# Kernel tuning notes

Measured on AMD Instinct MI355X. Metric: run time of the kernel, lower is better.

The kernel has to match this reference:

```python
import jax, jax.numpy as jnp
import numpy as np

NUM_HEADS = 8
HEAD_DIM = 128
ATTN_SCALE = 0.12


def _rotary_tables(T, head_dim, dtype=jnp.float32):
    # modded-nanogpt half-truncated RoPE: rotate only first half of freq slots
    quarter = head_dim // 4
    angular = (1.0 / 1024.0) ** jnp.linspace(0.0, 1.0, quarter, dtype=dtype)
    angular = jnp.concatenate([angular, jnp.zeros(quarter, dtype=dtype)])  # [head_dim//2]
    t = jnp.arange(T, dtype=dtype)
    theta = t[:, None] * angular[None, :]  # [T, head_dim//2]
    return jnp.cos(theta), jnp.sin(theta)


def _apply_rotary(x, cos, sin):
    # x: [B, T, H, D]; cos/sin: [T, D//2]
    x1, x2 = jnp.split(x, 2, axis=-1)
    c = cos[None, :, None, :]
    s = sin[None, :, None, :]
    y1 = x1 * c + x2 * s
    y2 = -x1 * s + x2 * c
    return jnp.concatenate([y1, y2], axis=-1)


def _rms_norm(x):
    eps = jnp.asarray(jnp.finfo(x.dtype).eps, x.dtype)
    var = jnp.mean(jnp.square(x), axis=-1, keepdims=True)
    return x * jax.lax.rsqrt(var + eps)


def setup_inputs() -> dict:
    key = jax.random.key(0)
    k1, k2, k3, k4, k5 = jax.random.split(key, 5)
    B, T, D = 1, 4096, 1024
    hdim = NUM_HEADS * HEAD_DIM
    std = 0.5 * D ** (-0.5)
    x = jax.random.normal(k1, (B, T, D), dtype=jnp.float32)
    ve = jax.random.normal(k2, (B, T, hdim), dtype=jnp.float32)
    qkv_w = jax.random.normal(k3, (3, hdim, D), dtype=jnp.float32) * std
    lambdas = jnp.array([0.5, 0.5], dtype=jnp.float32)
    c_proj_w = jax.random.normal(k5, (D, hdim), dtype=jnp.float32) * std
    return {"x": x, "ve": ve, "qkv_w": qkv_w, "lambdas": lambdas, "c_proj_w": c_proj_w}


def reference(x, ve, qkv_w, lambdas, c_proj_w):
    B, T, D = x.shape
    H, Hd = NUM_HEADS, HEAD_DIM
    # QKV projection: qkv_w [3, H*Hd, D]
    qkv = jnp.einsum('btd,ckd->btck', x, qkv_w)  # [B, T, 3, H*Hd]
    qkv = qkv.reshape(B, T, 3, H, Hd)
    q, k, v = qkv[:, :, 0], qkv[:, :, 1], qkv[:, :, 2]  # [B, T, H, Hd]
    # QK RMSNorm
    q = _rms_norm(q)
    k = _rms_norm(k)
    # RoPE
    cos, sin = _rotary_tables(T, Hd, dtype=x.dtype)
    q = _apply_rotary(q, cos, sin)
    k = _apply_rotary(k, cos, sin)
    # value-embedding lambda mix
    v = lambdas[0] * v + lambdas[1] * ve.reshape(B, T, H, Hd)
    # causal attention with fixed scale 0.12 (block-causal FlexAttention mask)
    scores = jnp.einsum('bthd,bshd->bhts', q, k) * ATTN_SCALE  # [B, H, T, T]
    causal = jnp.tril(jnp.ones((T, T), dtype=bool))
    scores = jnp.where(causal[None, None], scores, jnp.asarray(-jnp.inf, scores.dtype))
    probs = jax.nn.softmax(scores, axis=-1)
    y = jnp.einsum('bhts,bshd->bthd', probs, v)  # [B, T, H, Hd]
    y = y.reshape(B, T, H * Hd)
    return y @ c_proj_w.T  # [B, T, D]
```

## Files before the change

### kernel.cpp

```cpp
#include <hip/hip_runtime.h>

typedef __bf16 bf16;
typedef __bf16 bf16x8 __attribute__((ext_vector_type(8)));
typedef __bf16 bf16x4 __attribute__((ext_vector_type(4)));
typedef __bf16 bf16x2 __attribute__((ext_vector_type(2)));
typedef float f32x4 __attribute__((ext_vector_type(4)));
typedef float f32x16 __attribute__((ext_vector_type(16)));
typedef int i32x4 __attribute__((ext_vector_type(4)));

#define GLL16(gp, lp)                                                          \
  __builtin_amdgcn_global_load_lds(                                            \
      (const __attribute__((address_space(1))) unsigned int*)(gp),             \
      (__attribute__((address_space(3))) unsigned int*)(lp), 16, 0, 0)

__global__ __launch_bounds__(256) void cast3_f32_bf16(
    const float* __restrict__ a, bf16* __restrict__ oa, int na4,
    const float* __restrict__ b, bf16* __restrict__ ob, int nb4,
    const float* __restrict__ c, bf16* __restrict__ oc, int nc4) {
  int i = blockIdx.x * blockDim.x + threadIdx.x;
  int stride = gridDim.x * blockDim.x;
  int total = na4 + nb4 + nc4;
  for (; i < total; i += stride) {
    const float4* src;
    bf16x4* dst;
    int j = i;
    if (j < na4) {
      src = (const float4*)a + j; dst = (bf16x4*)oa + j;
    } else if ((j -= na4) < nb4) {
      src = (const float4*)b + j; dst = (bf16x4*)ob + j;
    } else {
      j -= nb4;
      src = (const float4*)c + j; dst = (bf16x4*)oc + j;
    }
    float4 v = *src;
    bf16x4 o;
    o[0] = (bf16)v.x; o[1] = (bf16)v.y; o[2] = (bf16)v.z; o[3] = (bf16)v.w;
    *dst = o;
  }
}

template <int K, int LDC, typename CT>
__global__ __launch_bounds__(256) void gemm_bt(
    const bf16* __restrict__ A, const bf16* __restrict__ B,
    CT* __restrict__ C) {
  __shared__ __align__(16) bf16 As[128 * 64];
  __shared__ __align__(16) bf16 Bs[128 * 64];
  const int tid  = threadIdx.x;
  const int lane = tid & 63;
  const int wave = tid >> 6;
  const int ln15 = lane & 15, quad = lane >> 4;
  const int wm = wave >> 1, wn = wave & 1;
  const int m0 = blockIdx.y * 128, n0 = blockIdx.x * 128;

  f32x4 acc[4][4] = {};

  for (int k0 = 0; k0 < K; k0 += 64) {
    __syncthreads();
#pragma unroll
    for (int j = 0; j < 4; ++j) {
      int gbase = j * 256 + wave * 64;
      int g = gbase + lane;
      int r = g >> 3, c = (g & 7) ^ (r & 7);
      GLL16(A + (size_t)(m0 + r) * K + k0 + c * 8, As + (size_t)gbase * 8);
    }
#pragma unroll
    for (int j = 0; j < 4; ++j) {
      int gbase = j * 256 + wave * 64;
      int g = gbase + lane;
      int r = g >> 3, c = (g & 7) ^ (r & 7);
      GLL16(B + (size_t)(n0 + r) * K + k0 + c * 8, Bs + (size_t)gbase * 8);
    }
    __syncthreads();
#pragma unroll
    for (int kk = 0; kk < 2; ++kk) {
      bf16x8 af[4], bfr[4];
#pragma unroll
      for (int mi = 0; mi < 4; ++mi) {
        int m = wm * 64 + mi * 16 + ln15;
        int cg = kk * 4 + quad;
        af[mi] = *(const bf16x8*)(As + (m * 8 + (cg ^ (m & 7))) * 8);
      }
#pragma unroll
      for (int ni = 0; ni < 4; ++ni) {
        int n = wn * 64 + ni * 16 + ln15;
        int cg = kk * 4 + quad;
        bfr[ni] = *(const bf16x8*)(Bs + (n * 8 + (cg ^ (n & 7))) * 8);
      }
#pragma unroll
      for (int mi = 0; mi < 4; ++mi)
#pragma unroll
        for (int ni = 0; ni < 4; ++ni)
          acc[mi][ni] = __builtin_amdgcn_mfma_f32_16x16x32_bf16(
              af[mi], bfr[ni], acc[mi][ni], 0, 0, 0);
    }
  }
#pragma unroll
  for (int mi = 0; mi < 4; ++mi)
#pragma unroll
    for (int ni = 0; ni < 4; ++ni)
#pragma unroll
      for (int r = 0; r < 4; ++r) {
        int row = m0 + wm * 64 + mi * 16 + quad * 4 + r;
        int col = n0 + wn * 64 + ni * 16 + ln15;
        C[(size_t)row * LDC + col] = (CT)acc[mi][ni][r];
      }
}

__global__ __launch_bounds__(256) void qkv_post(
    const bf16* __restrict__ qkv, const float* __restrict__ ve,
    const float* __restrict__ lambdas, bf16* __restrict__ qn,
    bf16* __restrict__ kn, bf16* __restrict__ vt) {
  const int h  = blockIdx.x;
  const int t0 = blockIdx.y * 64;
  const int tid = threadIdx.x;
  const int wave = tid >> 6, lane = tid & 63;
  __shared__ __align__(16) float tile[64][129];

  const int j = lane;
  float cth = 1.0f, sth = 0.0f;
  for (int i = 0; i < 16; ++i) {
    int t = t0 + wave * 16 + i;
    if (j < 32) {
      float ang = exp2f((float)j * (-10.0f / 31.0f));
      float th = (float)t * ang;
      __sincosf(th, &sth, &cth);
    }
#pragma unroll
    for (int qk = 0; qk < 2; ++qk) {
      const bf16* row = qkv + (size_t)t * 3072 + qk * 1024 + h * 128;
      float x1 = (float)row[j], x2 = (float)row[j + 64];
      float ss = x1 * x1 + x2 * x2;
#pragma unroll
      for (int m = 1; m < 64; m <<= 1) ss += __shfl_xor(ss, m, 64);
      float rinv = rsqrtf(ss * (1.0f / 128.0f) + 1.1920929e-7f);
      if (qk == 0) rinv *= 0.12f;
      float y1 = (x1 * cth + x2 * sth) * rinv;
      float y2 = (x2 * cth - x1 * sth) * rinv;
      bf16* orow = (qk == 0 ? qn : kn) + (size_t)t * 1024 + h * 128;
      orow[j] = (bf16)y1;
      orow[j + 64] = (bf16)y2;
    }
  }

  float l0 = lambdas[0], l1 = lambdas[1];
  for (int c = 0; c < 32; ++c) {
    int idx = c * 256 + tid;
    int d = idx & 127, tl = idx >> 7;
    int t = t0 + tl;
    float v = (float)qkv[(size_t)t * 3072 + 2048 + h * 128 + d];
    float vev = ve[(size_t)t * 1024 + h * 128 + d];
    tile[tl][d] = l0 * v + l1 * vev;
  }
  __syncthreads();
  for (int c = 0; c < 32; ++c) {
    int idx = c * 256 + tid;
    int tl = idx & 63, d = idx >> 6;
    vt[((size_t)(h * 128 + d)) * 4096 + t0 + tl] = (bf16)tile[tl][d];
  }
}

__global__ __launch_bounds__(256, 2) void flash_attn(
    const bf16* __restrict__ qn, const bf16* __restrict__ kn,
    const bf16* __restrict__ vt, bf16* __restrict__ y) {
  const int halfg = blockIdx.x >> 8;
  const int idx = blockIdx.x & 255;
  const int h = idx & 7;
  const int p = idx >> 3;
  const int qtile = halfg ? p : 63 - p;
  const int tid = threadIdx.x;
  const int wave = tid >> 6, lane = tid & 63;
  const int l31 = lane & 31, hl = lane >> 5;
  const int qi = wave >> 1, ki = wave & 1;

  __shared__ __align__(16) bf16 Ks[2][64 * 128];
  __shared__ __align__(16) bf16 Vs[2][128 * 64];
  __shared__ float rsb[2][2][32];

  const int q0 = qtile * 64;
  const int nkv = qtile + 1;
  const int qg = q0 + qi * 32 + l31;

  bf16x8 qf[8];
  {
    const bf16* qb = qn + (size_t)qg * 1024 + h * 128 + hl * 8;
#pragma unroll
    for (int f = 0; f < 8; ++f) qf[f] = *(const bf16x8*)(qb + f * 16);
  }

  f32x16 acc_o[4] = {};
  float rs = 0.0f;

  auto prefetch = [&](int kt, int buf) {
    const int kv0 = kt * 64;
    bf16* ks = &Ks[buf][0];
    bf16* vs = &Vs[buf][0];
#pragma unroll
    for (int jj = 0; jj < 4; ++jj) {
      int gbase = jj * 256 + wave * 64;
      int g = gbase + lane;
      int r = g >> 4, c = (g & 15) ^ (r & 15);
      GLL16(kn + (size_t)(kv0 + r) * 1024 + h * 128 + c * 8,
            ks + (size_t)gbase * 8);
    }
#pragma unroll
    for (int jj = 0; jj < 4; ++jj) {
      int gbase = jj * 256 + wave * 64;
      int g = gbase + lane;
      int d = g >> 3, c = (g & 7) ^ (d & 7);
      GLL16(vt + ((size_t)(h * 128 + d)) * 4096 + kv0 + c * 8,
            vs + (size_t)gbase * 8);
    }
  };

  prefetch(0, 0);

  for (int kt = 0; kt < nkv; ++kt) {
    const int kv0 = kt * 64;
    __syncthreads();
    if (kt + 1 < nkv) prefetch(kt + 1, (kt + 1) & 1);
    const bf16* ksb = &Ks[kt & 1][0];
    const bf16* vsb = &Vs[kt & 1][0];

    f32x16 accs = {};
    const int krow = ki * 32 + l31;
#pragma unroll
    for (int f = 0; f < 8; ++f) {
      bf16x8 a =
          *(const bf16x8*)(ksb + (krow * 16 + ((2 * f + hl) ^ (krow & 15))) * 8);
      accs = __builtin_amdgcn_mfma_f32_32x32x16_bf16(a, qf[f], accs, 0, 0, 0);
    }

    const bool diag = (kt == nkv - 1);
    float pe[16];
#pragma unroll
    for (int r = 0; r < 16; ++r) {
      int kvl = (r & 3) + 8 * (r >> 2) + 4 * hl;
      float v = __expf(accs[r]);
      if (diag && (kv0 + ki * 32 + kvl) > qg) v = 0.0f;
      rs += v;
      pe[r] = v;
    }
    int pk[8];
#pragma unroll
    for (int g = 0; g < 8; ++g) {
      bf16x2 t;
      t[0] = (bf16)pe[2 * g];
      t[1] = (bf16)pe[2 * g + 1];
      pk[g] = __builtin_bit_cast(int, t);
    }

    bf16x8 pf[2];
#pragma unroll
    for (int c = 0; c < 2; ++c) {
      int sh0 = __shfl_xor(pk[4 * c + 0], 32, 64);
      int sh1 = __shfl_xor(pk[4 * c + 1], 32, 64);
      int sh2 = __shfl_xor(pk[4 * c + 2], 32, 64);
      int sh3 = __shfl_xor(pk[4 * c + 3], 32, 64);
      int own0 = hl ? pk[4 * c + 2] : pk[4 * c + 0];
      int own1 = hl ? pk[4 * c + 3] : pk[4 * c + 1];
      int par0 = hl ? sh2 : sh0;
      int par1 = hl ? sh3 : sh1;
      i32x4 dv;
      dv[0] = hl ? par0 : own0;
      dv[1] = hl ? par1 : own1;
      dv[2] = hl ? own0 : par0;
      dv[3] = hl ? own1 : par1;
      pf[c] = __builtin_bit_cast(bf16x8, dv);
    }

#pragma unroll
    for (int dt = 0; dt < 4; ++dt) {
      int vrow = dt * 32 + l31;
#pragma unroll
      for (int c = 0; c < 2; ++c) {
        bf16x8 a = *(const bf16x8*)(
            vsb + (vrow * 8 + ((4 * ki + 2 * c + hl) ^ (vrow & 7))) * 8);
        acc_o[dt] =
            __builtin_amdgcn_mfma_f32_32x32x16_bf16(a, pf[c], acc_o[dt], 0, 0, 0);
      }
    }
  }

  rs += __shfl_xor(rs, 32, 64);
  __syncthreads();
  if (lane < 32) rsb[qi][ki][l31] = rs;
  float* ob = (float*)&Ks[0][0];
  if (ki == 1) {
#pragma unroll
    for (int dt = 0; dt < 4; ++dt)
#pragma unroll
      for (int r = 0; r < 16; ++r) {
        int d = dt * 32 + (r & 3) + 8 * (r >> 2) + 4 * hl;
        ob[qi * 4096 + l31 * 128 + d] = acc_o[dt][r];
      }
  }
  __syncthreads();
  if (ki == 0) {
    float inv = 1.0f / (rsb[qi][0][l31] + rsb[qi][1][l31]);
#pragma unroll
    for (int dt = 0; dt < 4; ++dt)
#pragma unroll
      for (int rg = 0; rg < 4; ++rg) {
        bf16x4 o;
#pragma unroll
        for (int j = 0; j < 4; ++j) {
          int r = rg * 4 + j;
          int d = dt * 32 + 4 * hl + 8 * rg + j;
          o[j] = (bf16)((acc_o[dt][r] + ob[qi * 4096 + l31 * 128 + d]) * inv);
        }
        *(bf16x4*)(y + (size_t)qg * 1024 + h * 128 + dt * 32 + 4 * hl + 8 * rg) = o;
      }
  }
}

extern "C" void kernel_launch(void* const* d_in, const int* in_sizes, int n_in,
                              void* d_out, int out_size, void* d_ws,
                              size_t ws_size, hipStream_t stream) {
  const float* x       = (const float*)d_in[0];
  const float* ve      = (const float*)d_in[1];
  const float* qkv_w   = (const float*)d_in[2];
  const float* lambdas = (const float*)d_in[3];
  const float* c_proj  = (const float*)d_in[4];
  float* out = (float*)d_out;

  char* ws = (char*)d_ws;
  bf16* qkv   = (bf16*)ws;
  bf16* xbf   = (bf16*)(ws + 25165824);
  bf16* wqkv  = (bf16*)(ws + 33554432);
  bf16* wproj = (bf16*)(ws + 39845888);
  bf16* qn    = (bf16*)(ws + 41943040);
  bf16* kn    = (bf16*)(ws + 50331648);
  bf16* vt    = (bf16*)(ws + 58720256);
  bf16* yb    = (bf16*)(ws + 67108864);

  cast3_f32_bf16<<<2048, 256, 0, stream>>>(x, xbf, 4194304 / 4, qkv_w, wqkv,
                                           3145728 / 4, c_proj, wproj,
                                           1048576 / 4);

  gemm_bt<1024, 3072, bf16><<<dim3(24, 32), 256, 0, stream>>>(xbf, wqkv, qkv);

  qkv_post<<<dim3(8, 64), 256, 0, stream>>>(qkv, ve, lambdas, qn, kn, vt);

  flash_attn<<<512, 256, 0, stream>>>(qn, kn, vt, yb);

  gemm_bt<1024, 1024, float><<<dim3(8, 32), 256, 0, stream>>>(yb, wproj, out);
}
```

Baseline: 252.3 us.

## Split attention KV range across two blocks and combine partials in separate kernel

Each query tile's causal KV range is now split into two halves processed by separate blocks, doubling the grid, with unnormalized fp32 partial outputs and row sums written to workspace. A new combine kernel adds the two partials and normalizes into bf16. Blocks are ordered longest-first so the heavy causal tiles start early. This is meant to improve load balance and occupancy. The cost is extra fp32 global traffic, an additional launch, and reuse of workspace regions freed earlier.

```diff
diff --git a/kernel.cpp b/kernel.cpp
--- a/kernel.cpp
+++ b/kernel.cpp
@@ -161,23 +161,40 @@
 
 __global__ __launch_bounds__(256, 2) void flash_attn(
     const bf16* __restrict__ qn, const bf16* __restrict__ kn,
-    const bf16* __restrict__ vt, bf16* __restrict__ y) {
-  const int halfg = blockIdx.x >> 8;
-  const int idx = blockIdx.x & 255;
-  const int h = idx & 7;
-  const int p = idx >> 3;
-  const int qtile = halfg ? p : 63 - p;
+    const bf16* __restrict__ vt, float* __restrict__ Op,
+    float* __restrict__ ls) {
+  const int id = blockIdx.x;
+  const int qtile = 63 - (id >> 4);
+  const int sub = id & 15;
+  const int h = sub >> 1;
+  const int half = sub & 1;
   const int tid = threadIdx.x;
   const int wave = tid >> 6, lane = tid & 63;
   const int l31 = lane & 31, hl = lane >> 5;
   const int qi = wave >> 1, ki = wave & 1;
 
-  __shared__ __align__(16) bf16 Ks[2][64 * 128];
-  __shared__ __align__(16) bf16 Vs[2][128 * 64];
+  __shared__ __align__(16) bf16 smem[4 * 64 * 128];
   __shared__ float rsb[2][2][32];
+  bf16* Ks = smem;
+  bf16* Vs = smem + 2 * 64 * 128;
 
   const int q0 = qtile * 64;
   const int nkv = qtile + 1;
+  const int half0 = (nkv + 1) >> 1;
+  const int kt_begin = half ? half0 : 0;
+  const int kt_end = half ? nkv : half0;
+  const int niter = kt_end - kt_begin;
+  const int pidx = (h * 64 + qtile) * 2 + half;
+
+  if (niter == 0) {
+    float4 z = {0.f, 0.f, 0.f, 0.f};
+    float* opb = Op + (size_t)pidx * 8192;
+#pragma unroll
+    for (int j = 0; j < 8; ++j) *(float4*)(opb + tid * 32 + j * 4) = z;
+    if (tid < 64) ls[pidx * 64 + tid] = 0.f;
+    return;
+  }
+
   const int qg = q0 + qi * 32 + l31;
 
   bf16x8 qf[8];
@@ -192,8 +209,8 @@
 
   auto prefetch = [&](int kt, int buf) {
     const int kv0 = kt * 64;
-    bf16* ks = &Ks[buf][0];
-    bf16* vs = &Vs[buf][0];
+    bf16* ks = Ks + buf * (64 * 128);
+    bf16* vs = Vs + buf * (128 * 64);
 #pragma unroll
     for (int jj = 0; jj < 4; ++jj) {
       int gbase = jj * 256 + wave * 64;
@@ -212,14 +229,15 @@
     }
   };
 
-  prefetch(0, 0);
-
-  for (int kt = 0; kt < nkv; ++kt) {
+  prefetch(kt_begin, 0);
+
+  for (int it = 0; it < niter; ++it) {
+    const int kt = kt_begin + it;
     const int kv0 = kt * 64;
     __syncthreads();
-    if (kt + 1 < nkv) prefetch(kt + 1, (kt + 1) & 1);
-    const bf16* ksb = &Ks[kt & 1][0];
-    const bf16* vsb = &Vs[kt & 1][0];
+    if (it + 1 < niter) prefetch(kt + 1, (it + 1) & 1);
+    const bf16* ksb = Ks + (it & 1) * (64 * 128);
+    const bf16* vsb = Vs + (it & 1) * (128 * 64);
 
     f32x16 accs = {};
     const int krow = ki * 32 + l31;
@@ -284,33 +302,56 @@
   rs += __shfl_xor(rs, 32, 64);
   __syncthreads();
   if (lane < 32) rsb[qi][ki][l31] = rs;
-  float* ob = (float*)&Ks[0][0];
+  float* ob = (float*)smem;
   if (ki == 1) {
 #pragma unroll
     for (int dt = 0; dt < 4; ++dt)
 #pragma unroll
       for (int r = 0; r < 16; ++r) {
         int d = dt * 32 + (r & 3) + 8 * (r >> 2) + 4 * hl;
-        ob[qi * 4096 + l31 * 128 + d] = acc_o[dt][r];
+        ob[(qi * 32 + l31) * 129 + d] = acc_o[dt][r];
       }
   }
   __syncthreads();
   if (ki == 0) {
-    float inv = 1.0f / (rsb[qi][0][l31] + rsb[qi][1][l31]);
+    float lsum = rsb[qi][0][l31] + rsb[qi][1][l31];
+    if (hl == 0) ls[pidx * 64 + qi * 32 + l31] = lsum;
+    float* opb = Op + (size_t)pidx * 8192 + (qi * 32 + l31) * 128;
 #pragma unroll
     for (int dt = 0; dt < 4; ++dt)
 #pragma unroll
       for (int rg = 0; rg < 4; ++rg) {
-        bf16x4 o;
-#pragma unroll
-        for (int j = 0; j < 4; ++j) {
-          int r = rg * 4 + j;
-          int d = dt * 32 + 4 * hl + 8 * rg + j;
-          o[j] = (bf16)((acc_o[dt][r] + ob[qi * 4096 + l31 * 128 + d]) * inv);
-        }
-        *(bf16x4*)(y + (size_t)qg * 1024 + h * 128 + dt * 32 + 4 * hl + 8 * rg) = o;
-      }
-  }
+        float4 o;
+        int d0 = dt * 32 + 4 * hl + 8 * rg;
+        o.x = acc_o[dt][rg * 4 + 0] + ob[(qi * 32 + l31) * 129 + d0 + 0];
+        o.y = acc_o[dt][rg * 4 + 1] + ob[(qi * 32 + l31) * 129 + d0 + 1];
+        o.z = acc_o[dt][rg * 4 + 2] + ob[(qi * 32 + l31) * 129 + d0 + 2];
+        o.w = acc_o[dt][rg * 4 + 3] + ob[(qi * 32 + l31) * 129 + d0 + 3];
+        *(float4*)(opb + d0) = o;
+      }
+  }
+}
+
+__global__ __launch_bounds__(256) void attn_combine(
+    const float* __restrict__ Op, const float* __restrict__ ls,
+    bf16* __restrict__ y) {
+  int gid = blockIdx.x * 256 + threadIdx.x;
+  int t = gid >> 8;
+  int c4 = gid & 255;
+  int qtile = t >> 6, ql = t & 63;
+  int h = c4 >> 5;
+  int d = (c4 & 31) * 4;
+  int pbase = (h * 64 + qtile) * 2;
+  const float4 o0 = *(const float4*)(Op + (size_t)pbase * 8192 + ql * 128 + d);
+  const float4 o1 =
+      *(const float4*)(Op + (size_t)(pbase + 1) * 8192 + ql * 128 + d);
+  float inv = 1.0f / (ls[pbase * 64 + ql] + ls[(pbase + 1) * 64 + ql]);
+  bf16x4 o;
+  o[0] = (bf16)((o0.x + o1.x) * inv);
+  o[1] = (bf16)((o0.y + o1.y) * inv);
+  o[2] = (bf16)((o0.z + o1.z) * inv);
+  o[3] = (bf16)((o0.w + o1.w) * inv);
+  *(bf16x4*)(y + (size_t)t * 1024 + h * 128 + d) = o;
 }
 
 extern "C" void kernel_launch(void* const* d_in, const int* in_sizes, int n_in,
@@ -332,6 +373,8 @@
   bf16* kn    = (bf16*)(ws + 50331648);
   bf16* vt    = (bf16*)(ws + 58720256);
   bf16* yb    = (bf16*)(ws + 67108864);
+  float* Op  = (float*)ws;
+  float* lsw = (float*)(ws + 33554432);
 
   cast3_f32_bf16<<<2048, 256, 0, stream>>>(x, xbf, 4194304 / 4, qkv_w, wqkv,
                                            3145728 / 4, c_proj, wproj,
@@ -341,7 +384,8 @@
 
   qkv_post<<<dim3(8, 64), 256, 0, stream>>>(qkv, ve, lambdas, qn, kn, vt);
 
-  flash_attn<<<512, 256, 0, stream>>>(qn, kn, vt, yb);
+  flash_attn<<<1024, 256, 0, stream>>>(qn, kn, vt, Op, lsw);
+  attn_combine<<<4096, 256, 0, stream>>>(Op, lsw, yb);
 
   gemm_bt<1024, 1024, float><<<dim3(8, 32), 256, 0, stream>>>(yb, wproj, out);
 }
```

After: 241.2 us. 1.05x faster.
